# Performance work log

Measured on AMD Instinct MI355X. Metric: run time of the kernel, lower is better.

Reference implementation:

```python
import jax, jax.numpy as jnp
import numpy as np

B, S, H = 32, 512, 768
N, E, P = 4096, 131072, 65536
HEADS1, C1 = 4, 128
HEADS2, C2 = 1, 64
NUM_REL, REL_HID = 6, 256
NER_HID, NER_LAB = 256, 9
LRELU_SLOPE = 0.2  # PyG GATConv default negative_slope
LN_EPS = 1e-5


def setup_inputs() -> dict:
    key = jax.random.key(0)
    ks = jax.random.split(key, 24)
    sc = 0.02
    inp = {
        'sequence_output': jax.random.normal(ks[0], (B, S, H), jnp.float32),
        'ent_start': jax.random.randint(ks[1], (N,), 0, S - 8),
        'ent_len': jax.random.randint(ks[2], (N,), 0, 8),
        'ent_batch': jax.random.randint(ks[3], (N,), 0, B),
        'edge_index': jax.random.randint(ks[4], (2, E), 0, N),
        'pair_idx': jax.random.randint(ks[5], (P, 2), 0, N),
        'W1': jax.random.normal(ks[6], (H, HEADS1 * C1), jnp.float32) * sc,
        'a_src1': jax.random.normal(ks[7], (HEADS1, C1), jnp.float32) * sc,
        'a_dst1': jax.random.normal(ks[8], (HEADS1, C1), jnp.float32) * sc,
        'b1': jnp.zeros((HEADS1 * C1,), jnp.float32),
        'W2': jax.random.normal(ks[9], (HEADS1 * C1, HEADS2 * C2), jnp.float32) * sc,
        'a_src2': jax.random.normal(ks[10], (HEADS2, C2), jnp.float32) * sc,
        'a_dst2': jax.random.normal(ks[11], (HEADS2, C2), jnp.float32) * sc,
        'b2': jnp.zeros((HEADS2 * C2,), jnp.float32),
        # 6 per-relation classifiers: Linear(128,256)+LN+ReLU+Linear(256,1)
        'relW1': jax.random.normal(ks[12], (NUM_REL, 2 * C2, REL_HID), jnp.float32) * sc,
        'relb1': jnp.zeros((NUM_REL, REL_HID), jnp.float32),
        'ln_g': jnp.ones((NUM_REL, REL_HID), jnp.float32),
        'ln_b': jnp.zeros((NUM_REL, REL_HID), jnp.float32),
        'relW2': jax.random.normal(ks[13], (NUM_REL, REL_HID, 1), jnp.float32) * sc,
        'relb2': jnp.zeros((NUM_REL, 1), jnp.float32),
        # NER head: Linear(768,256)+ReLU+Linear(256,9)
        'nerW1': jax.random.normal(ks[14], (H, NER_HID), jnp.float32) * sc,
        'nerb1': jnp.zeros((NER_HID,), jnp.float32),
        'nerW2': jax.random.normal(ks[15], (NER_HID, NER_LAB), jnp.float32) * sc,
        'nerb2': jnp.zeros((NER_LAB,), jnp.float32),
    }
    return inp


def _gat(x, src, dst, W, a_src, a_dst, b, heads, ch, n):
    # PyG GATConv: per-head linear, additive attention, softmax over incoming edges
    h = (x @ W).reshape(n, heads, ch)                      # [N,Hd,C]
    e_src = jnp.sum(h * a_src, axis=-1)                    # [N,Hd]
    e_dst = jnp.sum(h * a_dst, axis=-1)
    e = jax.nn.leaky_relu(e_src[src] + e_dst[dst], LRELU_SLOPE)  # [E,Hd]
    m = jax.ops.segment_max(e, dst, num_segments=n)
    ex = jnp.exp(e - m[dst])
    denom = jax.ops.segment_sum(ex, dst, num_segments=n)
    alpha = ex / denom[dst]                                # [E,Hd]
    out = jax.ops.segment_sum(alpha[:, :, None] * h[src], dst, num_segments=n)
    return out.reshape(n, heads * ch) + b


def reference(sequence_output, ent_start, ent_len, ent_batch, edge_index, pair_idx,
              W1, a_src1, a_dst1, b1, W2, a_src2, a_dst2, b2,
              relW1, relb1, ln_g, ln_b, relW2, relb2,
              nerW1, nerb1, nerW2, nerb2):
    n = ent_start.shape[0]
    # NER head on the full sequence
    ner_logits = jax.nn.relu(sequence_output @ nerW1 + nerb1) @ nerW2 + nerb2  # [B,S,9]
    # Entity-span mean pooling via exclusive prefix sums (inclusive span start..start+len)
    csum = jnp.cumsum(sequence_output, axis=1)
    csum = jnp.concatenate([jnp.zeros((B, 1, H), sequence_output.dtype), csum], axis=1)  # [B,S+1,H]
    ent_end = ent_start + ent_len
    span_sum = csum[ent_batch, ent_end + 1] - csum[ent_batch, ent_start]  # [N,H]
    x = span_sum / (ent_len + 1).astype(span_sum.dtype)[:, None]
    # add self loops (PyG GATConv default add_self_loops=True)
    loops = jnp.arange(n, dtype=edge_index.dtype)
    src = jnp.concatenate([edge_index[0], loops])
    dst = jnp.concatenate([edge_index[1], loops])
    x = _gat(x, src, dst, W1, a_src1, a_dst1, b1, HEADS1, C1, n)
    x = jax.nn.relu(x)  # dropout p=0.3 is identity in eval mode
    x = _gat(x, src, dst, W2, a_src2, a_dst2, b2, HEADS2, C2, n)  # [N,64]
    # Pair features: cat(x[e1], x[e2]) -> [P,128]
    pair_feat = jnp.concatenate([x[pair_idx[:, 0]], x[pair_idx[:, 1]]], axis=-1)
    # All 6 relation classifiers, vectorized over the relation dim
    hid = jnp.einsum('pf,rfk->rpk', pair_feat, relW1) + relb1[:, None, :]  # [6,P,256]
    mu = jnp.mean(hid, axis=-1, keepdims=True)
    var = jnp.mean(jnp.square(hid - mu), axis=-1, keepdims=True)
    hid = (hid - mu) * jax.lax.rsqrt(var + LN_EPS) * ln_g[:, None, :] + ln_b[:, None, :]
    hid = jax.nn.relu(hid)
    rel_logits = (jnp.einsum('rpk,rko->rpo', hid, relW2) + relb2[:, None, :])[..., 0]  # [6,P]
    return ner_logits, rel_logits
```

## Files before the change

kernel.cpp:

```cpp
#include <hip/hip_runtime.h>
#include <math.h>

#define LRELU 0.2f

constexpr int Bn = 32, Sn = 512, Hn = 768, Nn = 4096, En = 131072, Pn = 65536;
constexpr int ET = En + Nn;

typedef __attribute__((ext_vector_type(8))) short bf16x8;
typedef __attribute__((ext_vector_type(4))) float f32x4;

constexpr size_t OFF_X0  = 0;
constexpr size_t OFF_UV  = 0;
constexpr size_t OFF_H1  = 4194304;
constexpr size_t OFF_X1  = OFF_H1  + 2097152;
constexpr size_t OFF_H2  = OFF_X1  + 2097152;
constexpr size_t OFF_X2  = OFF_H2  + 262144;
constexpr size_t OFF_ES1 = OFF_X2  + 262144;
constexpr size_t OFF_ED1 = OFF_ES1 + 16384;
constexpr size_t OFF_ES2 = OFF_ED1 + 16384;
constexpr size_t OFF_ED2 = OFF_ES2 + 4096;
constexpr size_t OFF_ROW = OFF_ED2 + 4096;
constexpr size_t OFF_CUR = OFF_ROW + 4104;
constexpr size_t OFF_EDG = OFF_CUR + 4096;
constexpr size_t OFF_W1S = OFF_EDG + 135168;
constexpr size_t OFF_NW1S = OFF_W1S + 196608;
constexpr size_t OFF_W2S = OFF_NW1S + 98304;

__device__ __forceinline__ short f2bf(float f) {
  union { float f; unsigned u; } x; x.f = f;
  unsigned r = x.u + 0x7fff + ((x.u >> 16) & 1);
  return (short)(r >> 16);
}
__device__ __forceinline__ float bf2f(short s) {
  union { unsigned u; float f; } x;
  x.u = ((unsigned)(unsigned short)s) << 16;
  return x.f;
}

__global__ __launch_bounds__(256) void span_pool_k(
    const float* __restrict__ seq, const int* __restrict__ est,
    const int* __restrict__ eln, const int* __restrict__ ebt,
    float* __restrict__ x0) {
  int idx = blockIdx.x * 256 + threadIdx.x;
  if (idx >= Nn * (Hn / 4)) return;
  int e = idx / (Hn / 4);
  int c = (idx % (Hn / 4)) * 4;
  int s0 = est[e], L = eln[e] + 1, b = ebt[e];
  const float* p = seq + ((size_t)b * Sn + s0) * Hn + c;
  float ax = 0, ay = 0, az = 0, aw = 0;
  for (int i = 0; i < L; ++i) {
    float4 v = *(const float4*)(p + (size_t)i * Hn);
    ax += v.x; ay += v.y; az += v.z; aw += v.w;
  }
  float inv = 1.0f / (float)L;
  float4 o; o.x = ax * inv; o.y = ay * inv; o.z = az * inv; o.w = aw * inv;
  *(float4*)&x0[(size_t)e * Hn + c] = o;
}

template <int EPI, int NTW, int KC>
__global__ __launch_bounds__(256) void mfma_gemm_k(
    const float* __restrict__ A, const short* __restrict__ Bswz,
    float* __restrict__ C, const float* __restrict__ bias,
    int M, int K, int N) {
  constexpr int RS = KC + 8;
  __shared__ short at[64 * RS];
  int t = threadIdx.x;
  size_t rowb = (size_t)blockIdx.x * 64;
  int colb = blockIdx.y * (64 * NTW);
  int w = t >> 6, lane = t & 63, quad = lane >> 4, id = lane & 15;
  f32x4 acc[4][NTW];
#pragma unroll
  for (int mt = 0; mt < 4; ++mt)
#pragma unroll
    for (int nt = 0; nt < NTW; ++nt) acc[mt][nt] = (f32x4){0.f, 0.f, 0.f, 0.f};

  for (int k0 = 0; k0 < K; k0 += KC) {
    constexpr int CH = 64 * KC / 8 / 256;
#pragma unroll
    for (int i = 0; i < CH; ++i) {
      int cid = t + i * 256;
      int p = cid / (KC / 8), o8 = (cid % (KC / 8)) * 8;
      const float* src = &A[(rowb + p) * (size_t)K + k0 + o8];
      float4 v0 = *(const float4*)src;
      float4 v1 = *(const float4*)(src + 4);
      bf16x8 bv;
      bv[0] = f2bf(v0.x); bv[1] = f2bf(v0.y); bv[2] = f2bf(v0.z); bv[3] = f2bf(v0.w);
      bv[4] = f2bf(v1.x); bv[5] = f2bf(v1.y); bv[6] = f2bf(v1.z); bv[7] = f2bf(v1.w);
      *(bf16x8*)&at[p * RS + o8] = bv;
    }
    __syncthreads();
#pragma unroll
    for (int kk = 0; kk < KC / 32; ++kk) {
      bf16x8 af[4], bfr[NTW];
#pragma unroll
      for (int mt = 0; mt < 4; ++mt)
        af[mt] = *(const bf16x8*)&at[(mt * 16 + id) * RS + kk * 32 + quad * 8];
#pragma unroll
      for (int nt = 0; nt < NTW; ++nt) {
        int ntg = (colb >> 4) + w * NTW + nt;
        bfr[nt] = *(const bf16x8*)&Bswz[(((size_t)(k0 >> 5) + kk) * (N >> 4) + ntg) * 512 + lane * 8];
      }
#pragma unroll
      for (int mt = 0; mt < 4; ++mt)
#pragma unroll
        for (int nt = 0; nt < NTW; ++nt)
          acc[mt][nt] = __builtin_amdgcn_mfma_f32_16x16x32_bf16(af[mt], bfr[nt], acc[mt][nt], 0, 0, 0);
    }
    __syncthreads();
  }
#pragma unroll
  for (int nt = 0; nt < NTW; ++nt) {
    int col = colb + w * (16 * NTW) + nt * 16 + id;
#pragma unroll
    for (int mt = 0; mt < 4; ++mt) {
#pragma unroll
      for (int reg = 0; reg < 4; ++reg) {
        size_t row = rowb + mt * 16 + quad * 4 + reg;
        float v = acc[mt][nt][reg];
        if (EPI == 3) {
          int r = col >> 9, rem = col & 511;
          if (rem < 256) v += bias[(r << 8) + rem];
          ((short*)C)[((size_t)r * Nn + row) * 512 + rem] = f2bf(v);
        } else if (EPI == 2) {
          ((short*)C)[row * (size_t)N + col] = f2bf(v);
        } else {
          C[row * (size_t)N + col] = v;
        }
      }
    }
  }
}

__global__ __launch_bounds__(256) void ner_fused_k(
    const float* __restrict__ A, const short* __restrict__ Bswz,
    const float* __restrict__ W2, const float* __restrict__ b1,
    const float* __restrict__ b2, float* __restrict__ out) {
  constexpr int K = 768;
  constexpr int RS = 136, HS = 264, WS = 260;
  __shared__ short at[64 * RS];
  __shared__ short hid[64 * HS];
  __shared__ float w2t[9 * WS];
  __shared__ float b2l[9];
  int t = threadIdx.x;
  size_t rowb = (size_t)blockIdx.x * 64;
  for (int u = t; u < 2304; u += 256) {
    int k = u / 9, jj = u % 9;
    w2t[jj * WS + k] = W2[u];
  }
  if (t < 9) b2l[t] = b2[t];
  int w = t >> 6, lane = t & 63, quad = lane >> 4, id = lane & 15;
  f32x4 acc[4][4];
#pragma unroll
  for (int mt = 0; mt < 4; ++mt)
#pragma unroll
    for (int nt = 0; nt < 4; ++nt) acc[mt][nt] = (f32x4){0.f, 0.f, 0.f, 0.f};

  for (int k0 = 0; k0 < K; k0 += 128) {
#pragma unroll
    for (int i = 0; i < 4; ++i) {
      int cid = t + i * 256;
      int p = cid >> 4, o8 = (cid & 15) * 8;
      const float* src = &A[(rowb + p) * (size_t)K + k0 + o8];
      float4 v0 = *(const float4*)src;
      float4 v1 = *(const float4*)(src + 4);
      bf16x8 bv;
      bv[0] = f2bf(v0.x); bv[1] = f2bf(v0.y); bv[2] = f2bf(v0.z); bv[3] = f2bf(v0.w);
      bv[4] = f2bf(v1.x); bv[5] = f2bf(v1.y); bv[6] = f2bf(v1.z); bv[7] = f2bf(v1.w);
      *(bf16x8*)&at[p * RS + o8] = bv;
    }
    __syncthreads();
#pragma unroll
    for (int kk = 0; kk < 4; ++kk) {
      bf16x8 af[4], bfr[4];
#pragma unroll
      for (int mt = 0; mt < 4; ++mt)
        af[mt] = *(const bf16x8*)&at[(mt * 16 + id) * RS + kk * 32 + quad * 8];
#pragma unroll
      for (int nt = 0; nt < 4; ++nt) {
        int ntg = w * 4 + nt;
        bfr[nt] = *(const bf16x8*)&Bswz[(((size_t)(k0 >> 5) + kk) * 16 + ntg) * 512 + lane * 8];
      }
#pragma unroll
      for (int mt = 0; mt < 4; ++mt)
#pragma unroll
        for (int nt = 0; nt < 4; ++nt)
          acc[mt][nt] = __builtin_amdgcn_mfma_f32_16x16x32_bf16(af[mt], bfr[nt], acc[mt][nt], 0, 0, 0);
    }
    __syncthreads();
  }
#pragma unroll
  for (int nt = 0; nt < 4; ++nt) {
    int col = w * 64 + nt * 16 + id;
    float bb = b1[col];
#pragma unroll
    for (int mt = 0; mt < 4; ++mt)
#pragma unroll
      for (int reg = 0; reg < 4; ++reg) {
        int row = mt * 16 + quad * 4 + reg;
        hid[row * HS + col] = f2bf(fmaxf(acc[mt][nt][reg] + bb, 0.f));
      }
  }
  __syncthreads();
  for (int u = t; u < 576; u += 256) {
    int row = u / 9, jj = u % 9;
    const short* hp = &hid[row * HS];
    const float* wp = &w2t[jj * WS];
    float a = 0.f;
#pragma unroll
    for (int k8 = 0; k8 < 256; k8 += 8) {
      bf16x8 hv = *(const bf16x8*)&hp[k8];
      float4 w0 = *(const float4*)&wp[k8];
      float4 w1 = *(const float4*)&wp[k8 + 4];
      a += bf2f(hv[0]) * w0.x + bf2f(hv[1]) * w0.y + bf2f(hv[2]) * w0.z + bf2f(hv[3]) * w0.w;
      a += bf2f(hv[4]) * w1.x + bf2f(hv[5]) * w1.y + bf2f(hv[6]) * w1.z + bf2f(hv[7]) * w1.w;
    }
    out[(rowb + row) * 9 + jj] = a + b2l[jj];
  }
}

__device__ __forceinline__ void swz_store(short* __restrict__ o, int k, int n, int N, float v) {
  int kk = k >> 5, quad = (k >> 3) & 3, j = k & 7, ntg = n >> 4, id = n & 15;
  o[(((size_t)kk * (N >> 4)) + ntg) * 512 + (quad * 16 + id) * 8 + j] = f2bf(v);
}

__global__ void swz_all_k(const float* __restrict__ W1, const float* __restrict__ nW1,
                          const float* __restrict__ W2, short* __restrict__ w1s,
                          short* __restrict__ nw1s, short* __restrict__ w2s) {
  int i = blockIdx.x * 256 + threadIdx.x;
  if (i < 768 * 512) {
    swz_store(w1s, i / 512, i % 512, 512, W1[i]);
  } else if (i < 768 * 512 + 768 * 256) {
    int i2 = i - 768 * 512;
    swz_store(nw1s, i2 / 256, i2 % 256, 256, nW1[i2]);
  } else if (i < 768 * 512 + 768 * 256 + 512 * 64) {
    int i2 = i - (768 * 512 + 768 * 256);
    swz_store(w2s, i2 / 64, i2 % 64, 64, W2[i2]);
  }
}

__global__ void swz_uv_k(const float* __restrict__ rW1, short* __restrict__ o) {
  int i = blockIdx.x * 256 + threadIdx.x;
  if (i >= 6 * 128 * 256) return;
  int n = i & 255, k = (i >> 8) & 127, r = i >> 15;
  int c = r * 512 + (k >> 6) * 256 + n;
  int kr = k & 63;
  int kk = kr >> 5, quad = (kr >> 3) & 3, j = kr & 7, ntg = c >> 4, id = c & 15;
  o[(((size_t)kk * 192) + ntg) * 512 + (quad * 16 + id) * 8 + j] = f2bf(rW1[i]);
}

template <int HD, int C>
__global__ __launch_bounds__(256) void coef_b_k(
    const short* __restrict__ h, const float* __restrict__ a_src,
    const float* __restrict__ a_dst, float* __restrict__ es, float* __restrict__ ed) {
  int idx = blockIdx.x * 256 + threadIdx.x;
  if (idx >= Nn * HD) return;
  int n = idx / HD, hd = idx % HD;
  const short* hp = h + (size_t)n * HD * C + hd * C;
  const float* sp = a_src + hd * C;
  const float* dp = a_dst + hd * C;
  float s = 0, d = 0;
  for (int c = 0; c < C; c += 8) {
    bf16x8 v = *(const bf16x8*)(hp + c);
#pragma unroll
    for (int k = 0; k < 8; ++k) {
      float f = bf2f(v[k]);
      s += f * sp[c + k];
      d += f * dp[c + k];
    }
  }
  es[idx] = s; ed[idx] = d;
}

__global__ void zero_k(int* __restrict__ p, int n) {
  int i = blockIdx.x * 256 + threadIdx.x;
  if (i < n) p[i] = 0;
}

__global__ void count_k(const int* __restrict__ eidx, int* __restrict__ cnt) {
  int i = blockIdx.x * 256 + threadIdx.x;
  if (i >= ET) return;
  int dst = (i < En) ? eidx[En + i] : (i - En);
  atomicAdd(&cnt[dst], 1);
}

__global__ __launch_bounds__(256) void scan_k(int* cnt_cur, int* rowoff) {
  __shared__ int s[256];
  int t = threadIdx.x;
  int loc[16]; int run = 0; int base = t * 16;
#pragma unroll
  for (int i = 0; i < 16; ++i) { loc[i] = run; run += cnt_cur[base + i]; }
  s[t] = run;
  __syncthreads();
  for (int off = 1; off < 256; off <<= 1) {
    int v = (t >= off) ? s[t - off] : 0;
    __syncthreads();
    s[t] += v;
    __syncthreads();
  }
  int offset = (t > 0) ? s[t - 1] : 0;
#pragma unroll
  for (int i = 0; i < 16; ++i) {
    int o = offset + loc[i];
    rowoff[base + i] = o;
    cnt_cur[base + i] = o;
  }
  if (t == 255) rowoff[4096] = s[255];
}

__global__ void scatter_k(const int* __restrict__ eidx, int* __restrict__ cur,
                          int* __restrict__ esrc) {
  int i = blockIdx.x * 256 + threadIdx.x;
  if (i >= ET) return;
  int s, d;
  if (i < En) { s = eidx[i]; d = eidx[En + i]; } else { s = d = i - En; }
  int pos = atomicAdd(&cur[d], 1);
  esrc[pos] = s;
}

__global__ void pcount_k(const int* __restrict__ pidx, int* __restrict__ cnt) {
  int p = blockIdx.x * 256 + threadIdx.x;
  if (p < Pn) atomicAdd(&cnt[pidx[2 * p]], 1);
}

__global__ void pscatter3_k(const int* __restrict__ pidx, int* __restrict__ cur,
                            int4* __restrict__ plist) {
  int p = blockIdx.x * 256 + threadIdx.x;
  if (p >= Pn) return;
  int i = pidx[2 * p], j = pidx[2 * p + 1];
  int pos = atomicAdd(&cur[i], 1);
  plist[pos] = make_int4(i, j, p, 0);
}

template <int HD, int C, bool RELU>
__global__ __launch_bounds__(256) void gat_agg_k(
    const short* __restrict__ h, const float* __restrict__ es,
    const float* __restrict__ ed, const int* __restrict__ row_off,
    const int* __restrict__ eslist, const float* __restrict__ bias,
    float* __restrict__ xout) {
  constexpr int HDC = HD * C, OCT = HDC / 8, JS = 256 / OCT;
  constexpr int CAP = 320;
  __shared__ float red[256];
  __shared__ float mxs[HD], dns[HD];
  __shared__ float exc[CAP * HD];
  __shared__ float part[JS * HDC];
  int n = blockIdx.x, t = threadIdx.x;
  int ro = row_off[n], deg = row_off[n + 1] - ro;
  int hd = t % HD, ei = t / HD;
  constexpr int ES = 256 / HD;
  float edv = ed[n * HD + hd];
  float pm = -3.402823466e38f;
  for (int j = ei; j < deg; j += ES) {
    int s = eslist[ro + j];
    float e = es[s * HD + hd] + edv;
    e = (e > 0.f) ? e : LRELU * e;
    pm = fmaxf(pm, e);
  }
  red[t] = pm;
  __syncthreads();
  for (int off = 128; off >= HD; off >>= 1) {
    if (t < off) red[t] = fmaxf(red[t], red[t + off]);
    __syncthreads();
  }
  if (t < HD) mxs[t] = red[t];
  __syncthreads();
  float mx = mxs[hd];
  float ps = 0.f;
  for (int j = ei; j < deg; j += ES) {
    int s = eslist[ro + j];
    float e = es[s * HD + hd] + edv;
    e = (e > 0.f) ? e : LRELU * e;
    float ex = __expf(e - mx);
    if (j < CAP) exc[j * HD + hd] = ex;
    ps += ex;
  }
  red[t] = ps;
  __syncthreads();
  for (int off = 128; off >= HD; off >>= 1) {
    if (t < off) red[t] += red[t + off];
    __syncthreads();
  }
  if (t < HD) dns[t] = red[t];
  __syncthreads();
  int oc = t % OCT, js = t / OCT;
  int hh = oc / (C / 8);
  float mxh = mxs[hh], edh = ed[n * HD + hh];
  float a[8];
#pragma unroll
  for (int k = 0; k < 8; ++k) a[k] = 0.f;
  for (int j = js; j < deg; j += JS) {
    int s = eslist[ro + j];
    float ex;
    if (j < CAP) ex = exc[j * HD + hh];
    else {
      float e = es[s * HD + hh] + edh;
      e = (e > 0.f) ? e : LRELU * e;
      ex = __expf(e - mxh);
    }
    bf16x8 hv = *(const bf16x8*)&h[(size_t)s * HDC + oc * 8];
#pragma unroll
    for (int k = 0; k < 8; ++k) a[k] += ex * bf2f(hv[k]);
  }
#pragma unroll
  for (int k = 0; k < 8; ++k) part[js * HDC + oc * 8 + k] = a[k];
  __syncthreads();
  for (int c = t; c < HDC; c += 256) {
    float sum = 0.f;
#pragma unroll
    for (int q = 0; q < JS; ++q) sum += part[q * HDC + c];
    int hh2 = c / C;
    float v = sum / dns[hh2] + bias[c];
    if (RELU) v = fmaxf(v, 0.f);
    xout[(size_t)n * HDC + c] = v;
  }
}

__global__ __launch_bounds__(256) void pair_rel_k(
    const short* __restrict__ UV, const int4* __restrict__ plist,
    const float* __restrict__ lng, const float* __restrict__ lnb,
    const float* __restrict__ rW2, const float* __restrict__ rb2,
    float* __restrict__ out) {
  int t = threadIdx.x;
  int r = blockIdx.y;
  int w = t >> 6, lane = t & 63;
  int pg = lane >> 4, l16 = lane & 15;
  float g[16], bb[16], wv[16];
  int cb = r * 256 + l16 * 16;
#pragma unroll
  for (int q = 0; q < 4; ++q) {
    *(float4*)&g[q * 4]  = *(const float4*)&lng[cb + q * 4];
    *(float4*)&bb[q * 4] = *(const float4*)&lnb[cb + q * 4];
    *(float4*)&wv[q * 4] = *(const float4*)&rW2[cb + q * 4];
  }
  float rb2v = rb2[r];
  const short* UVr = UV + (size_t)r * Nn * 512;
  int qbase = blockIdx.x * 256 + w * 64;
  for (int it = 0; it < 16; ++it) {
    int4 ijp = plist[qbase + it * 4 + pg];
    const short* up = &UVr[(size_t)ijp.x * 512 + l16 * 16];
    const short* vp = &UVr[(size_t)ijp.y * 512 + 256 + l16 * 16];
    bf16x8 u0 = *(const bf16x8*)up, u1 = *(const bf16x8*)(up + 8);
    bf16x8 v0 = *(const bf16x8*)vp, v1 = *(const bf16x8*)(vp + 8);
    float hv[16], s1 = 0.f, s2 = 0.f;
#pragma unroll
    for (int cc = 0; cc < 8; ++cc) {
      float h = bf2f(u0[cc]) + bf2f(v0[cc]);
      hv[cc] = h; s1 += h; s2 += h * h;
    }
#pragma unroll
    for (int cc = 0; cc < 8; ++cc) {
      float h = bf2f(u1[cc]) + bf2f(v1[cc]);
      hv[8 + cc] = h; s1 += h; s2 += h * h;
    }
#pragma unroll
    for (int off = 1; off < 16; off <<= 1) {
      s1 += __shfl_xor(s1, off, 64);
      s2 += __shfl_xor(s2, off, 64);
    }
    float mu = s1 * (1.f / 256.f);
    float var = s2 * (1.f / 256.f) - mu * mu;
    float rs = rsqrtf(var + 1e-5f);
    float pv = 0.f;
#pragma unroll
    for (int cc = 0; cc < 16; ++cc) {
      float v = (hv[cc] - mu) * rs * g[cc] + bb[cc];
      v = fmaxf(v, 0.f);
      pv += v * wv[cc];
    }
#pragma unroll
    for (int off = 1; off < 16; off <<= 1) pv += __shfl_xor(pv, off, 64);
    if (l16 == 0) out[(size_t)r * Pn + ijp.z] = pv + rb2v;
  }
}

extern "C" void kernel_launch(void* const* d_in, const int* in_sizes, int n_in,
                              void* d_out, int out_size, void* d_ws, size_t ws_size,
                              hipStream_t stream) {
  const float* seq = (const float*)d_in[0];
  const int* est = (const int*)d_in[1];
  const int* eln = (const int*)d_in[2];
  const int* ebt = (const int*)d_in[3];
  const int* eidx = (const int*)d_in[4];
  const int* pidx = (const int*)d_in[5];
  const float* W1 = (const float*)d_in[6];
  const float* as1 = (const float*)d_in[7];
  const float* ad1 = (const float*)d_in[8];
  const float* b1 = (const float*)d_in[9];
  const float* W2 = (const float*)d_in[10];
  const float* as2 = (const float*)d_in[11];
  const float* ad2 = (const float*)d_in[12];
  const float* b2 = (const float*)d_in[13];
  const float* rW1 = (const float*)d_in[14];
  const float* rb1 = (const float*)d_in[15];
  const float* lng = (const float*)d_in[16];
  const float* lnb = (const float*)d_in[17];
  const float* rW2 = (const float*)d_in[18];
  const float* rb2 = (const float*)d_in[19];
  const float* nW1 = (const float*)d_in[20];
  const float* nb1 = (const float*)d_in[21];
  const float* nW2 = (const float*)d_in[22];
  const float* nb2 = (const float*)d_in[23];
  float* out = (float*)d_out;
  float* ws = (float*)d_ws;

  float* x0 = ws + OFF_X0;
  short* uv = (short*)(ws + OFF_UV);
  short* h1 = (short*)(ws + OFF_H1);
  float* x1 = ws + OFF_X1;
  short* h2 = (short*)(ws + OFF_H2);
  short* uvw = (short*)(ws + OFF_H2);
  float* x2 = ws + OFF_X2;
  float* es1 = ws + OFF_ES1;
  float* ed1 = ws + OFF_ED1;
  float* es2 = ws + OFF_ES2;
  float* ed2 = ws + OFF_ED2;
  int* rowoff = (int*)(ws + OFF_ROW);
  int* cur = (int*)(ws + OFF_CUR);
  int* edg = (int*)(ws + OFF_EDG);
  short* w1s = (short*)(ws + OFF_W1S);
  short* nw1s = (short*)(ws + OFF_NW1S);
  short* w2s = (short*)(ws + OFF_W2S);
  int* prow = (int*)(ws + OFF_X1);
  int* pcur = (int*)(ws + OFF_X1 + 4104);
  int4* plist = (int4*)(ws + OFF_X1 + 8208);

  zero_k<<<16, 256, 0, stream>>>(cur, Nn);
  count_k<<<(ET + 255) / 256, 256, 0, stream>>>(eidx, cur);
  scan_k<<<1, 256, 0, stream>>>(cur, rowoff);
  scatter_k<<<(ET + 255) / 256, 256, 0, stream>>>(eidx, cur, edg);
  swz_all_k<<<(768 * 512 + 768 * 256 + 512 * 64 + 255) / 256, 256, 0, stream>>>(
      W1, nW1, W2, w1s, nw1s, w2s);

  span_pool_k<<<Nn * (Hn / 4) / 256, 256, 0, stream>>>(seq, est, eln, ebt, x0);

  mfma_gemm_k<2, 2, 128><<<dim3(Nn / 64, 512 / 128), 256, 0, stream>>>(x0, w1s, (float*)h1, nullptr, Nn, Hn, 512);
  coef_b_k<4, 128><<<(Nn * 4) / 256, 256, 0, stream>>>(h1, as1, ad1, es1, ed1);
  gat_agg_k<4, 128, true><<<Nn, 256, 0, stream>>>(h1, es1, ed1, rowoff, edg, b1, x1);

  mfma_gemm_k<2, 1, 128><<<dim3(Nn / 64, 1), 256, 0, stream>>>(x1, w2s, (float*)h2, nullptr, Nn, 512, 64);

  zero_k<<<16, 256, 0, stream>>>(pcur, Nn);
  pcount_k<<<Pn / 256, 256, 0, stream>>>(pidx, pcur);
  scan_k<<<1, 256, 0, stream>>>(pcur, prow);
  pscatter3_k<<<Pn / 256, 256, 0, stream>>>(pidx, pcur, plist);

  coef_b_k<1, 64><<<(Nn + 255) / 256, 256, 0, stream>>>(h2, as2, ad2, es2, ed2);
  gat_agg_k<1, 64, false><<<Nn, 256, 0, stream>>>(h2, es2, ed2, rowoff, edg, b2, x2);

  swz_uv_k<<<(6 * 128 * 256) / 256, 256, 0, stream>>>(rW1, uvw);
  mfma_gemm_k<3, 2, 64><<<dim3(Nn / 64, 3072 / 128), 256, 0, stream>>>(x2, uvw, (float*)uv, rb1, Nn, 64, 3072);
  pair_rel_k<<<dim3(Pn / 256, 6), 256, 0, stream>>>(uv, plist, lng, lnb, rW2, rb2,
                                                    out + (size_t)Bn * Sn * 9);

  ner_fused_k<<<(Bn * Sn) / 64, 256, 0, stream>>>(seq, nw1s, nW2, nb1, nb2, out);
}
```

Measured before the change: 369.0 us.

## Drop pair sorting, use node-major UV layout and software-prefetch pair gathers

Removes the pair count/scan/scatter preprocessing that grouped pairs by first entity, and has pair_rel_k read pair indices directly in original order. The UV GEMM epilogue now writes a node-major [N,3072] bf16 layout instead of relation-major, so each pair's six relation rows share one contiguous row per node. The pair kernel processes 32 pairs per wave with a one-step register prefetch of the next pair's gathers, and launches twice as many blocks. This removes four small launches and an atomic scatter, at the cost of losing the locality the sorted order gave for the first-entity gathers.

```diff
diff --git a/kernel.cpp b/kernel.cpp
--- a/kernel.cpp
+++ b/kernel.cpp
@@ -117,10 +117,10 @@
       for (int reg = 0; reg < 4; ++reg) {
         size_t row = rowb + mt * 16 + quad * 4 + reg;
         float v = acc[mt][nt][reg];
-        if (EPI == 3) {
+        if (EPI == 4) {
           int r = col >> 9, rem = col & 511;
           if (rem < 256) v += bias[(r << 8) + rem];
-          ((short*)C)[((size_t)r * Nn + row) * 512 + rem] = f2bf(v);
+          ((short*)C)[row * (size_t)N + col] = f2bf(v);
         } else if (EPI == 2) {
           ((short*)C)[row * (size_t)N + col] = f2bf(v);
         } else {
@@ -315,20 +315,6 @@
   if (i < En) { s = eidx[i]; d = eidx[En + i]; } else { s = d = i - En; }
   int pos = atomicAdd(&cur[d], 1);
   esrc[pos] = s;
-}
-
-__global__ void pcount_k(const int* __restrict__ pidx, int* __restrict__ cnt) {
-  int p = blockIdx.x * 256 + threadIdx.x;
-  if (p < Pn) atomicAdd(&cnt[pidx[2 * p]], 1);
-}
-
-__global__ void pscatter3_k(const int* __restrict__ pidx, int* __restrict__ cur,
-                            int4* __restrict__ plist) {
-  int p = blockIdx.x * 256 + threadIdx.x;
-  if (p >= Pn) return;
-  int i = pidx[2 * p], j = pidx[2 * p + 1];
-  int pos = atomicAdd(&cur[i], 1);
-  plist[pos] = make_int4(i, j, p, 0);
 }
 
 template <int HD, int C, bool RELU>
@@ -415,7 +401,7 @@
 }
 
 __global__ __launch_bounds__(256) void pair_rel_k(
-    const short* __restrict__ UV, const int4* __restrict__ plist,
+    const short* __restrict__ UV, const int* __restrict__ pidx,
     const float* __restrict__ lng, const float* __restrict__ lnb,
     const float* __restrict__ rW2, const float* __restrict__ rb2,
     float* __restrict__ out) {
@@ -432,23 +418,35 @@
     *(float4*)&wv[q * 4] = *(const float4*)&rW2[cb + q * 4];
   }
   float rb2v = rb2[r];
-  const short* UVr = UV + (size_t)r * Nn * 512;
-  int qbase = blockIdx.x * 256 + w * 64;
-  for (int it = 0; it < 16; ++it) {
-    int4 ijp = plist[qbase + it * 4 + pg];
-    const short* up = &UVr[(size_t)ijp.x * 512 + l16 * 16];
-    const short* vp = &UVr[(size_t)ijp.y * 512 + 256 + l16 * 16];
-    bf16x8 u0 = *(const bf16x8*)up, u1 = *(const bf16x8*)(up + 8);
-    bf16x8 v0 = *(const bf16x8*)vp, v1 = *(const bf16x8*)(vp + 8);
+  size_t roff = (size_t)r * 512 + l16 * 16;
+  int pbase = blockIdx.x * 128 + w * 32;
+  int p = pbase + pg;
+  int2 ij = *(const int2*)&pidx[2 * p];
+  const short* up = &UV[(size_t)ij.x * 3072 + roff];
+  const short* vp = &UV[(size_t)ij.y * 3072 + roff + 256];
+  bf16x8 u0 = *(const bf16x8*)up, u1 = *(const bf16x8*)(up + 8);
+  bf16x8 v0 = *(const bf16x8*)vp, v1 = *(const bf16x8*)(vp + 8);
+#pragma unroll
+  for (int it = 0; it < 8; ++it) {
+    bf16x8 cu0 = u0, cu1 = u1, cv0 = v0, cv1 = v1;
+    int cp = p;
+    if (it < 7) {
+      p = pbase + (it + 1) * 4 + pg;
+      ij = *(const int2*)&pidx[2 * p];
+      up = &UV[(size_t)ij.x * 3072 + roff];
+      vp = &UV[(size_t)ij.y * 3072 + roff + 256];
+      u0 = *(const bf16x8*)up; u1 = *(const bf16x8*)(up + 8);
+      v0 = *(const bf16x8*)vp; v1 = *(const bf16x8*)(vp + 8);
+    }
     float hv[16], s1 = 0.f, s2 = 0.f;
 #pragma unroll
     for (int cc = 0; cc < 8; ++cc) {
-      float h = bf2f(u0[cc]) + bf2f(v0[cc]);
+      float h = bf2f(cu0[cc]) + bf2f(cv0[cc]);
       hv[cc] = h; s1 += h; s2 += h * h;
     }
 #pragma unroll
     for (int cc = 0; cc < 8; ++cc) {
-      float h = bf2f(u1[cc]) + bf2f(v1[cc]);
+      float h = bf2f(cu1[cc]) + bf2f(cv1[cc]);
       hv[8 + cc] = h; s1 += h; s2 += h * h;
     }
 #pragma unroll
@@ -468,7 +466,7 @@
     }
 #pragma unroll
     for (int off = 1; off < 16; off <<= 1) pv += __shfl_xor(pv, off, 64);
-    if (l16 == 0) out[(size_t)r * Pn + ijp.z] = pv + rb2v;
+    if (l16 == 0) out[(size_t)r * Pn + cp] = pv + rb2v;
   }
 }
 
@@ -519,9 +517,6 @@
   short* w1s = (short*)(ws + OFF_W1S);
   short* nw1s = (short*)(ws + OFF_NW1S);
   short* w2s = (short*)(ws + OFF_W2S);
-  int* prow = (int*)(ws + OFF_X1);
-  int* pcur = (int*)(ws + OFF_X1 + 4104);
-  int4* plist = (int4*)(ws + OFF_X1 + 8208);
 
   zero_k<<<16, 256, 0, stream>>>(cur, Nn);
   count_k<<<(ET + 255) / 256, 256, 0, stream>>>(eidx, cur);
@@ -537,18 +532,12 @@
   gat_agg_k<4, 128, true><<<Nn, 256, 0, stream>>>(h1, es1, ed1, rowoff, edg, b1, x1);
 
   mfma_gemm_k<2, 1, 128><<<dim3(Nn / 64, 1), 256, 0, stream>>>(x1, w2s, (float*)h2, nullptr, Nn, 512, 64);
-
-  zero_k<<<16, 256, 0, stream>>>(pcur, Nn);
-  pcount_k<<<Pn / 256, 256, 0, stream>>>(pidx, pcur);
-  scan_k<<<1, 256, 0, stream>>>(pcur, prow);
-  pscatter3_k<<<Pn / 256, 256, 0, stream>>>(pidx, pcur, plist);
-
   coef_b_k<1, 64><<<(Nn + 255) / 256, 256, 0, stream>>>(h2, as2, ad2, es2, ed2);
   gat_agg_k<1, 64, false><<<Nn, 256, 0, stream>>>(h2, es2, ed2, rowoff, edg, b2, x2);
 
   swz_uv_k<<<(6 * 128 * 256) / 256, 256, 0, stream>>>(rW1, uvw);
-  mfma_gemm_k<3, 2, 64><<<dim3(Nn / 64, 3072 / 128), 256, 0, stream>>>(x2, uvw, (float*)uv, rb1, Nn, 64, 3072);
-  pair_rel_k<<<dim3(Pn / 256, 6), 256, 0, stream>>>(uv, plist, lng, lnb, rW2, rb2,
+  mfma_gemm_k<4, 2, 64><<<dim3(Nn / 64, 3072 / 128), 256, 0, stream>>>(x2, uvw, (float*)uv, rb1, Nn, 64, 3072);
+  pair_rel_k<<<dim3(Pn / 128, 6), 256, 0, stream>>>(uv, pidx, lng, lnb, rW2, rb2,
                                                     out + (size_t)Bn * Sn * 9);
 
   ner_fused_k<<<(Bn * Sn) / 64, 256, 0, stream>>>(seq, nw1s, nW2, nb1, nb2, out);
```

New measurement: 335.1 us. -9.2%, faster.
